# Kernel tuning notes

Measured on AMD Instinct MI355X. Metric: run time of the kernel, lower is better.

Reference implementation:

```python
import jax, jax.numpy as jnp
import numpy as np

HID = 768          # args.hidden_size
LSTM2 = 768        # args.lstm_dim * 2
SCALE = HID ** -0.5


def _cross_attn(q_in, kv_in, Wq, bq, Wk, bk, Wv, bv):
    # Linear projections (weights stored as [in, out])
    Q = q_in @ Wq + bq            # [B, Sq, H]
    K = kv_in @ Wk + bk           # [B, Sk, H]
    V = kv_in @ Wv + bv           # [B, Sk, H]
    attn = jnp.einsum('bqh,bkh->bqk', Q, K) * SCALE
    attn = jax.nn.softmax(attn, axis=-1)
    return jnp.einsum('bqk,bkh->bqh', attn, V)


def setup_inputs() -> dict:
    key = jax.random.key(0)
    ks = jax.random.split(key, 14)
    B, Ssyn, Ssem = 4, 4096, 2048
    syntactic_feat = jax.random.normal(ks[0], (B, Ssyn, LSTM2), jnp.float32)
    semantic_feat = jax.random.normal(ks[1], (B, Ssem, HID), jnp.float32)

    def lin(k, fan_in, fan_out):
        kw, kb = jax.random.split(k)
        bound = 1.0 / np.sqrt(fan_in)
        W = jax.random.uniform(kw, (fan_in, fan_out), jnp.float32, -bound, bound)
        b = jax.random.uniform(kb, (fan_out,), jnp.float32, -bound, bound)
        return W, b

    # syntax_to_semantic: query_dim=HID, key_dim=LSTM2
    Wq1, bq1 = lin(ks[2], HID, HID)
    Wk1, bk1 = lin(ks[3], LSTM2, HID)
    Wv1, bv1 = lin(ks[4], LSTM2, HID)
    # semantic_to_syntax: query_dim=LSTM2, key_dim=HID
    Wq2, bq2 = lin(ks[5], LSTM2, HID)
    Wk2, bk2 = lin(ks[6], HID, HID)
    Wv2, bv2 = lin(ks[7], HID, HID)
    return dict(syntactic_feat=syntactic_feat, semantic_feat=semantic_feat,
                Wq1=Wq1, bq1=bq1, Wk1=Wk1, bk1=bk1, Wv1=Wv1, bv1=bv1,
                Wq2=Wq2, bq2=bq2, Wk2=Wk2, bk2=bk2, Wv2=Wv2, bv2=bv2)


def reference(syntactic_feat, semantic_feat,
              Wq1, bq1, Wk1, bk1, Wv1, bv1,
              Wq2, bq2, Wk2, bk2, Wv2, bv2):
    # enhanced_semantic: queries from semantic, keys/values from syntactic
    enhanced_semantic = _cross_attn(semantic_feat, syntactic_feat,
                                    Wq1, bq1, Wk1, bk1, Wv1, bv1)
    # enhanced_syntax: queries from syntactic, keys/values from semantic
    enhanced_syntax = _cross_attn(syntactic_feat, semantic_feat,
                                  Wq2, bq2, Wk2, bk2, Wv2, bv2)
    return enhanced_semantic, enhanced_syntax
```

## Files before the change

kernel.cpp:

```cpp
#include <hip/hip_runtime.h>
#include <stdint.h>


typedef unsigned short u16;
typedef __attribute__((ext_vector_type(8))) __bf16 bf16x8;
typedef __attribute__((ext_vector_type(4))) float f32x4;

__device__ __forceinline__ float bf2f(u16 u) {
  union { unsigned int i; float f; } x; x.i = ((unsigned int)u) << 16; return x.f;
}
__device__ __forceinline__ u16 f2bf(float f) {
  union { float f; unsigned int i; } x; x.f = f;
  unsigned int i = x.i;
  i += 0x7fffu + ((i >> 16) & 1u);
  return (u16)(i >> 16);
}

__device__ __forceinline__ void cp16(void* lds, const void* g) {
  __builtin_amdgcn_global_load_lds((__attribute__((address_space(1))) void*)g,
                                   (__attribute__((address_space(3))) void*)lds,
                                   16, 0, 0);
}

struct GemmDesc {
  const u16* A; const u16* Bt; const float* bias; void* C;
  long sA, sB, sC;
  int K, lda, ldb, ldc;
  int gx, gy;
  int start;
  int mode, outf;
  float scale;
};
struct GemmPack { GemmDesc d[6]; int nd; };

__global__ __launch_bounds__(256)
void gemm_multi_kernel(GemmPack p)
{
  __shared__ __align__(16) u16 Asl[128 * 32];
  __shared__ __align__(16) u16 Bsl[128 * 32];

  int seg = 0;
#pragma unroll
  for (int t = 1; t < 6; ++t)
    if (t < p.nd && (int)blockIdx.x >= p.d[t].start) seg = t;
  const GemmDesc& g = p.d[seg];
  const int local = (int)blockIdx.x - g.start;
  const int pxy = g.gx * g.gy;
  const int bz = local / pxy;
  const int rem = local - bz * pxy;
  const int by = rem / g.gx;
  const int bx = rem - by * g.gx;

  const int tid  = threadIdx.x;
  const int lane = tid & 63;
  const int wave = tid >> 6;
  const int l15  = lane & 15;
  const int quad = lane >> 4;
  const int mw   = (wave >> 1) * 64;
  const int nw   = (wave & 1) * 64;

  const char* Ab = (const char*)(g.A + (long)bz * g.sA + (long)bx * 128 * g.lda);
  const char* Bb = (const char*)(g.Bt + (long)bz * g.sB + (long)by * 128 * g.ldb);

  const int o   = wave * 1024 + lane * 16;
  const int mst = o >> 6;
  const int off = o & 63;
  char* ldsA = (char*)Asl + wave * 1024;
  char* ldsB = (char*)Bsl + wave * 1024;
  const long ldaB = (long)g.lda * 2;
  const long ldbB = (long)g.ldb * 2;
  const char* pa0 = Ab + (long)mst * ldaB + off;
  const char* pb0 = Bb + (long)mst * ldbB + off;

  f32x4 acc[4][4];
  {
    f32x4 zz = {0.f, 0.f, 0.f, 0.f};
#pragma unroll
    for (int i = 0; i < 4; ++i)
#pragma unroll
      for (int j = 0; j < 4; ++j) acc[i][j] = zz;
  }

  const int nk = g.K >> 5;
  for (int kk = 0; kk < nk; ++kk) {
    const long kb = (long)kk << 6;
    cp16(ldsA,        pa0 + kb);
    cp16(ldsA + 4096, pa0 + kb + 64 * ldaB);
    cp16(ldsB,        pb0 + kb);
    cp16(ldsB + 4096, pb0 + kb + 64 * ldbB);
    __syncthreads();

    bf16x8 a[4], b[4];
    const bf16x8* As8 = (const bf16x8*)Asl;
    const bf16x8* Bs8 = (const bf16x8*)Bsl;
#pragma unroll
    for (int i = 0; i < 4; ++i) a[i] = As8[(mw + i * 16 + l15) * 4 + quad];
#pragma unroll
    for (int j = 0; j < 4; ++j) b[j] = Bs8[(nw + j * 16 + l15) * 4 + quad];
#pragma unroll
    for (int i = 0; i < 4; ++i)
#pragma unroll
      for (int j = 0; j < 4; ++j)
        acc[i][j] = __builtin_amdgcn_mfma_f32_16x16x32_bf16(a[i], b[j], acc[i][j], 0, 0, 0);
    __syncthreads();
  }

  const int brow = bx * 128 + mw + quad * 4;
  const int bcol = by * 128 + nw + l15;
  float cb[4];
  if (g.mode == 1) {
#pragma unroll
    for (int j = 0; j < 4; ++j) cb[j] = g.bias[bcol + j * 16];
  }
#pragma unroll
  for (int i = 0; i < 4; ++i) {
    const int r0 = brow + i * 16;
    float rb[4];
    if (g.mode == 2) {
#pragma unroll
      for (int r = 0; r < 4; ++r) rb[r] = g.bias[r0 + r];
    }
#pragma unroll
    for (int j = 0; j < 4; ++j) {
      const int col = bcol + j * 16;
#pragma unroll
      for (int r = 0; r < 4; ++r) {
        float x = acc[i][j][r] * g.scale;
        if (g.mode == 1) x += cb[j];
        if (g.mode == 2) x += rb[r];
        const long idx = (long)bz * g.sC + (long)(r0 + r) * g.ldc + col;
        if (g.outf) ((float*)g.C)[idx] = x;
        else        ((u16*)g.C)[idx] = f2bf(x);
      }
    }
  }
}

__global__ __launch_bounds__(256)
void cvt2_bf16_kernel(const float* __restrict__ sa, u16* __restrict__ da, int n8a,
                      const float* __restrict__ sb, u16* __restrict__ db, int n8b)
{
  int idx = blockIdx.x * 256 + threadIdx.x;
  const float* src; u16* dst; int i;
  if (idx < n8a) { src = sa; dst = da; i = idx; }
  else           { src = sb; dst = db; i = idx - n8a; if (i >= n8b) return; }
  const float4* s4 = (const float4*)src;
  float4 a = s4[i * 2], b = s4[i * 2 + 1];
  uint4 o;
  o.x = (unsigned int)f2bf(a.x) | ((unsigned int)f2bf(a.y) << 16);
  o.y = (unsigned int)f2bf(a.z) | ((unsigned int)f2bf(a.w) << 16);
  o.z = (unsigned int)f2bf(b.x) | ((unsigned int)f2bf(b.y) << 16);
  o.w = (unsigned int)f2bf(b.z) | ((unsigned int)f2bf(b.w) << 16);
  ((uint4*)dst)[i] = o;
}

__global__ void transpose6_kernel(const float* s0, const float* s1, const float* s2,
                                  const float* s3, const float* s4, const float* s5,
                                  u16* d0, u16* d1, u16* d2,
                                  u16* d3, u16* d4, u16* d5)
{
  __shared__ float t[32][33];
  const float* src; u16* dst;
  switch (blockIdx.z) {
    case 0: src = s0; dst = d0; break;
    case 1: src = s1; dst = d1; break;
    case 2: src = s2; dst = d2; break;
    case 3: src = s3; dst = d3; break;
    case 4: src = s4; dst = d4; break;
    default: src = s5; dst = d5; break;
  }
  const int tx = threadIdx.x, ty = threadIdx.y;
  const int x = blockIdx.x * 32 + tx;
  const int y0 = blockIdx.y * 32;
#pragma unroll
  for (int j = 0; j < 32; j += 8) t[ty + j][tx] = src[(long)(y0 + ty + j) * 768 + x];
  __syncthreads();
  const int x2 = y0 + tx;
#pragma unroll
  for (int j = 0; j < 32; j += 8)
    dst[(long)(blockIdx.x * 32 + ty + j) * 768 + x2] = f2bf(t[tx][ty + j]);
}

template <int NV>
__global__ __launch_bounds__(256)
void softmax_kernel(u16* S)
{
  __shared__ float red[8];
  const int tid  = threadIdx.x;
  const int lane = tid & 63;
  const int wave = tid >> 6;
  uint4* p4 = (uint4*)(S + (long)blockIdx.x * (NV * 256));

  uint4 ld[NV / 8];
#pragma unroll
  for (int c = 0; c < NV / 8; ++c) ld[c] = p4[tid + c * 256];
  float v[NV];
#pragma unroll
  for (int c = 0; c < NV / 8; ++c) {
    unsigned int w[4] = {ld[c].x, ld[c].y, ld[c].z, ld[c].w};
#pragma unroll
    for (int q = 0; q < 4; ++q) {
      v[c * 8 + q * 2]     = bf2f((u16)(w[q] & 0xffffu));
      v[c * 8 + q * 2 + 1] = bf2f((u16)(w[q] >> 16));
    }
  }

  float m = -1e30f;
#pragma unroll
  for (int i = 0; i < NV; ++i) m = fmaxf(m, v[i]);
#pragma unroll
  for (int off = 32; off > 0; off >>= 1) m = fmaxf(m, __shfl_xor(m, off, 64));
  if (lane == 0) red[wave] = m;
  __syncthreads();
  m = fmaxf(fmaxf(red[0], red[1]), fmaxf(red[2], red[3]));

  float s = 0.f;
#pragma unroll
  for (int i = 0; i < NV; ++i) { v[i] = __expf(v[i] - m); s += v[i]; }
#pragma unroll
  for (int off = 32; off > 0; off >>= 1) s += __shfl_xor(s, off, 64);
  if (lane == 0) red[4 + wave] = s;
  __syncthreads();
  s = (red[4] + red[5]) + (red[6] + red[7]);
  const float inv = 1.0f / s;

#pragma unroll
  for (int c = 0; c < NV / 8; ++c) {
    unsigned int w[4];
#pragma unroll
    for (int q = 0; q < 4; ++q) {
      const u16 lo = f2bf(v[c * 8 + q * 2] * inv);
      const u16 hi = f2bf(v[c * 8 + q * 2 + 1] * inv);
      w[q] = (unsigned int)lo | ((unsigned int)hi << 16);
    }
    uint4 st; st.x = w[0]; st.y = w[1]; st.z = w[2]; st.w = w[3];
    p4[tid + c * 256] = st;
  }
}


static GemmDesc mkdesc(const void* A, const void* Bt, const float* bias, void* C,
                       long sA, long sB, long sC, int K, int lda, int ldb, int ldc,
                       int M, int N, int nb, int start, int mode, int outf, float scale)
{
  GemmDesc d;
  d.A = (const u16*)A; d.Bt = (const u16*)Bt; d.bias = bias; d.C = C;
  d.sA = sA; d.sB = sB; d.sC = sC;
  d.K = K; d.lda = lda; d.ldb = ldb; d.ldc = ldc;
  d.gx = M / 128; d.gy = N / 128; d.start = start;
  d.mode = mode; d.outf = outf; d.scale = scale;
  (void)nb;
  return d;
}

extern "C" void kernel_launch(void* const* d_in, const int* in_sizes, int n_in,
                              void* d_out, int out_size, void* d_ws, size_t ws_size,
                              hipStream_t stream)
{
  (void)in_sizes; (void)n_in; (void)out_size; (void)ws_size;
  const float* syn = (const float*)d_in[0];
  const float* sem = (const float*)d_in[1];
  const float* W[6]    = {(const float*)d_in[2], (const float*)d_in[4],  (const float*)d_in[6],
                          (const float*)d_in[8], (const float*)d_in[10], (const float*)d_in[12]};
  const float* bias[6] = {(const float*)d_in[3], (const float*)d_in[5],  (const float*)d_in[7],
                          (const float*)d_in[9], (const float*)d_in[11], (const float*)d_in[13]};
  float* out = (float*)d_out;

  u16* ws   = (u16*)d_ws;
  u16* WT   = ws;
  u16* synb = ws + 3538944;
  u16* semb = ws + 16121856;
  u16* S1   = ws;
  u16* K1   = ws + 33554432;
  u16* Q1   = ws + 46137344;
  u16* S2   = ws + 33554432;
  u16* V1T  = ws + 67108864;
  u16* V2T  = ws + 79691776;
  u16* Q2   = (u16*)(out + 6291456);
  u16* K2   = Q2 + 12582912;

  const float SC = 0.036084391824351615f;

  cvt2_bf16_kernel<<<dim3(9216), dim3(256), 0, stream>>>(
      syn, synb, 1572864, sem, semb, 786432);

  transpose6_kernel<<<dim3(24, 24, 6), dim3(32, 8, 1), 0, stream>>>(
      W[0], W[1], W[2], W[3], W[4], W[5],
      WT + 0 * 589824, WT + 1 * 589824, WT + 2 * 589824,
      WT + 3 * 589824, WT + 4 * 589824, WT + 5 * 589824);

  {
    GemmPack p; p.nd = 6;
    p.d[0] = mkdesc(synb, WT + 1 * 589824, bias[1], K1, 0, 0, 0,
                    768, 768, 768, 768, 16384, 768, 1, 0, 1, 0, 1.f);
    p.d[1] = mkdesc(synb, WT + 3 * 589824, bias[3], Q2, 0, 0, 0,
                    768, 768, 768, 768, 16384, 768, 1, 768, 1, 0, 1.f);
    p.d[2] = mkdesc(WT + 2 * 589824, synb, bias[2], V1T, 0, 0, 0,
                    768, 768, 768, 16384, 768, 16384, 1, 1536, 2, 0, 1.f);
    p.d[3] = mkdesc(semb, WT + 0 * 589824, bias[0], Q1, 0, 0, 0,
                    768, 768, 768, 768, 8192, 768, 1, 2304, 1, 0, 1.f);
    p.d[4] = mkdesc(semb, WT + 4 * 589824, bias[4], K2, 0, 0, 0,
                    768, 768, 768, 768, 8192, 768, 1, 2688, 1, 0, 1.f);
    p.d[5] = mkdesc(WT + 5 * 589824, semb, bias[5], V2T, 0, 0, 0,
                    768, 768, 768, 8192, 768, 8192, 1, 3072, 2, 0, 1.f);
    gemm_multi_kernel<<<dim3(3456), dim3(256), 0, stream>>>(p);
  }

  {
    GemmPack p; p.nd = 1;
    p.d[0] = mkdesc(Q1, K1, nullptr, S1,
                    1572864L, 3145728L, 8388608L,
                    768, 768, 768, 4096, 2048, 4096, 4, 0, 0, 0, SC);
    gemm_multi_kernel<<<dim3(2048), dim3(256), 0, stream>>>(p);
  }

  softmax_kernel<16><<<dim3(8192), dim3(256), 0, stream>>>(S1);

  {
    GemmPack p; p.nd = 2;
    p.d[0] = mkdesc(S1, V1T, nullptr, out,
                    8388608L, 4096L, 1572864L,
                    4096, 4096, 16384, 768, 2048, 768, 4, 0, 0, 1, 1.f);
    p.d[1] = mkdesc(Q2, K2, nullptr, S2,
                    3145728L, 1572864L, 8388608L,
                    768, 768, 768, 2048, 4096, 2048, 4, 384, 0, 0, SC);
    gemm_multi_kernel<<<dim3(2432), dim3(256), 0, stream>>>(p);
  }

  softmax_kernel<8><<<dim3(16384), dim3(256), 0, stream>>>(S2);

  {
    GemmPack p; p.nd = 1;
    p.d[0] = mkdesc(S2, V2T, nullptr, out + 6291456,
                    8388608L, 2048L, 3145728L,
                    2048, 2048, 8192, 768, 4096, 768, 4, 0, 0, 1, 1.f);
    gemm_multi_kernel<<<dim3(768), dim3(256), 0, stream>>>(p);
  }
}
```

Measured before the change: 650.3 us.

## Swizzle GEMM LDS layout, batch both score GEMMs and softmaxes, merge PV GEMMs

```diff
diff --git a/kernel.cpp b/kernel.cpp
--- a/kernel.cpp
+++ b/kernel.cpp
@@ -64,13 +64,24 @@
 
   const int o   = wave * 1024 + lane * 16;
   const int mst = o >> 6;
-  const int off = o & 63;
+  const int cl  = (o >> 4) & 3;
+  const int sst = (mst + (mst >> 2)) & 3;
+  const int off = (cl ^ sst) << 4;
   char* ldsA = (char*)Asl + wave * 1024;
   char* ldsB = (char*)Bsl + wave * 1024;
   const long ldaB = (long)g.lda * 2;
   const long ldbB = (long)g.ldb * 2;
   const char* pa0 = Ab + (long)mst * ldaB + off;
   const char* pb0 = Bb + (long)mst * ldbB + off;
+
+  int ia[4], ib[4];
+#pragma unroll
+  for (int i = 0; i < 4; ++i) {
+    const int m = mw + i * 16 + l15;
+    ia[i] = m * 4 + (quad ^ ((m + (m >> 2)) & 3));
+    const int n = nw + i * 16 + l15;
+    ib[i] = n * 4 + (quad ^ ((n + (n >> 2)) & 3));
+  }
 
   f32x4 acc[4][4];
   {
@@ -94,9 +105,9 @@
     const bf16x8* As8 = (const bf16x8*)Asl;
     const bf16x8* Bs8 = (const bf16x8*)Bsl;
 #pragma unroll
-    for (int i = 0; i < 4; ++i) a[i] = As8[(mw + i * 16 + l15) * 4 + quad];
-#pragma unroll
-    for (int j = 0; j < 4; ++j) b[j] = Bs8[(nw + j * 16 + l15) * 4 + quad];
+    for (int i = 0; i < 4; ++i) a[i] = As8[ia[i]];
+#pragma unroll
+    for (int j = 0; j < 4; ++j) b[j] = Bs8[ib[j]];
 #pragma unroll
     for (int i = 0; i < 4; ++i)
 #pragma unroll
@@ -182,14 +193,13 @@
 }
 
 template <int NV>
-__global__ __launch_bounds__(256)
-void softmax_kernel(u16* S)
+__device__ __forceinline__ void softmax_row(u16* row)
 {
   __shared__ float red[8];
   const int tid  = threadIdx.x;
   const int lane = tid & 63;
   const int wave = tid >> 6;
-  uint4* p4 = (uint4*)(S + (long)blockIdx.x * (NV * 256));
+  uint4* p4 = (uint4*)row;
 
   uint4 ld[NV / 8];
 #pragma unroll
@@ -238,10 +248,17 @@
   }
 }
 
+__global__ __launch_bounds__(256)
+void softmax_both_kernel(u16* S1, u16* S2)
+{
+  if (blockIdx.x < 8192) softmax_row<16>(S1 + (long)blockIdx.x * 4096);
+  else                   softmax_row<8>(S2 + (long)(blockIdx.x - 8192) * 2048);
+}
+
 
 static GemmDesc mkdesc(const void* A, const void* Bt, const float* bias, void* C,
                        long sA, long sB, long sC, int K, int lda, int ldb, int ldc,
-                       int M, int N, int nb, int start, int mode, int outf, float scale)
+                       int M, int N, int start, int mode, int outf, float scale)
 {
   GemmDesc d;
   d.A = (const u16*)A; d.Bt = (const u16*)Bt; d.bias = bias; d.C = C;
@@ -249,7 +266,6 @@
   d.K = K; d.lda = lda; d.ldb = ldb; d.ldc = ldc;
   d.gx = M / 128; d.gy = N / 128; d.start = start;
   d.mode = mode; d.outf = outf; d.scale = scale;
-  (void)nb;
   return d;
 }
 
@@ -267,17 +283,19 @@
   float* out = (float*)d_out;
 
   u16* ws   = (u16*)d_ws;
-  u16* WT   = ws;
-  u16* synb = ws + 3538944;
-  u16* semb = ws + 16121856;
   u16* S1   = ws;
-  u16* K1   = ws + 33554432;
-  u16* Q1   = ws + 46137344;
+  u16* synb = ws;
+  u16* semb = ws + 12582912;
+  u16* WT   = ws + 18874368;
   u16* S2   = ws + 33554432;
   u16* V1T  = ws + 67108864;
-  u16* V2T  = ws + 79691776;
-  u16* Q2   = (u16*)(out + 6291456);
-  u16* K2   = Q2 + 12582912;
+  u16* Q1   = ws + 79691776;
+  u16* V2Tc = ws + 79691776;
+  u16* K1  = (u16*)out;
+  u16* o1  = (u16*)(out + 6291456);
+  u16* Q2  = o1;
+  u16* K2  = o1 + 12582912;
+  u16* V2T = o1 + 18874368;
 
   const float SC = 0.036084391824351615f;
 
@@ -292,48 +310,43 @@
   {
     GemmPack p; p.nd = 6;
     p.d[0] = mkdesc(synb, WT + 1 * 589824, bias[1], K1, 0, 0, 0,
-                    768, 768, 768, 768, 16384, 768, 1, 0, 1, 0, 1.f);
+                    768, 768, 768, 768, 16384, 768, 0, 1, 0, 1.f);
     p.d[1] = mkdesc(synb, WT + 3 * 589824, bias[3], Q2, 0, 0, 0,
-                    768, 768, 768, 768, 16384, 768, 1, 768, 1, 0, 1.f);
+                    768, 768, 768, 768, 16384, 768, 768, 1, 0, 1.f);
     p.d[2] = mkdesc(WT + 2 * 589824, synb, bias[2], V1T, 0, 0, 0,
-                    768, 768, 768, 16384, 768, 16384, 1, 1536, 2, 0, 1.f);
+                    768, 768, 768, 16384, 768, 16384, 1536, 2, 0, 1.f);
     p.d[3] = mkdesc(semb, WT + 0 * 589824, bias[0], Q1, 0, 0, 0,
-                    768, 768, 768, 768, 8192, 768, 1, 2304, 1, 0, 1.f);
+                    768, 768, 768, 768, 8192, 768, 2304, 1, 0, 1.f);
     p.d[4] = mkdesc(semb, WT + 4 * 589824, bias[4], K2, 0, 0, 0,
-                    768, 768, 768, 768, 8192, 768, 1, 2688, 1, 0, 1.f);
+                    768, 768, 768, 768, 8192, 768, 2688, 1, 0, 1.f);
     p.d[5] = mkdesc(WT + 5 * 589824, semb, bias[5], V2T, 0, 0, 0,
-                    768, 768, 768, 8192, 768, 8192, 1, 3072, 2, 0, 1.f);
+                    768, 768, 768, 8192, 768, 8192, 3072, 2, 0, 1.f);
     gemm_multi_kernel<<<dim3(3456), dim3(256), 0, stream>>>(p);
   }
 
   {
-    GemmPack p; p.nd = 1;
+    GemmPack p; p.nd = 2;
     p.d[0] = mkdesc(Q1, K1, nullptr, S1,
                     1572864L, 3145728L, 8388608L,
-                    768, 768, 768, 4096, 2048, 4096, 4, 0, 0, 0, SC);
-    gemm_multi_kernel<<<dim3(2048), dim3(256), 0, stream>>>(p);
-  }
-
-  softmax_kernel<16><<<dim3(8192), dim3(256), 0, stream>>>(S1);
+                    768, 768, 768, 4096, 2048, 4096, 0, 0, 0, SC);
+    p.d[1] = mkdesc(Q2, K2, nullptr, S2,
+                    3145728L, 1572864L, 8388608L,
+                    768, 768, 768, 2048, 4096, 2048, 2048, 0, 0, SC);
+    gemm_multi_kernel<<<dim3(4096), dim3(256), 0, stream>>>(p);
+  }
+
+  softmax_both_kernel<<<dim3(24576), dim3(256), 0, stream>>>(S1, S2);
+
+  hipMemcpyAsync(V2Tc, V2T, 12582912, hipMemcpyDeviceToDevice, stream);
 
   {
     GemmPack p; p.nd = 2;
     p.d[0] = mkdesc(S1, V1T, nullptr, out,
                     8388608L, 4096L, 1572864L,
-                    4096, 4096, 16384, 768, 2048, 768, 4, 0, 0, 1, 1.f);
-    p.d[1] = mkdesc(Q2, K2, nullptr, S2,
-                    3145728L, 1572864L, 8388608L,
-                    768, 768, 768, 2048, 4096, 2048, 4, 384, 0, 0, SC);
-    gemm_multi_kernel<<<dim3(2432), dim3(256), 0, stream>>>(p);
-  }
-
-  softmax_kernel<8><<<dim3(16384), dim3(256), 0, stream>>>(S2);
-
-  {
-    GemmPack p; p.nd = 1;
-    p.d[0] = mkdesc(S2, V2T, nullptr, out + 6291456,
+                    4096, 4096, 16384, 768, 2048, 768, 0, 0, 1, 1.f);
+    p.d[1] = mkdesc(S2, V2Tc, nullptr, out + 6291456,
                     8388608L, 2048L, 3145728L,
-                    2048, 2048, 8192, 768, 4096, 768, 4, 0, 0, 1, 1.f);
-    gemm_multi_kernel<<<dim3(768), dim3(256), 0, stream>>>(p);
-  }
-}
+                    2048, 2048, 8192, 768, 4096, 768, 384, 0, 1, 1.f);
+    gemm_multi_kernel<<<dim3(1152), dim3(256), 0, stream>>>(p);
+  }
+}
```

Result: faster. 633.7 us (-2.5%).
